# Kernel tuning notes

Measured on AMD Instinct MI355X. Metric: run time of the kernel, lower is better.

The kernel has to match this reference:

```python
import jax, jax.numpy as jnp
import numpy as np

B, S, D = 2, 2048, 1024
H = 16
HD = D // H  # 64
SCALE = HD ** -0.5


def setup_inputs() -> dict:
    key = jax.random.key(0)
    k1, k2, k3 = jax.random.split(key, 3)
    x = jax.random.normal(k1, (B, S, D), dtype=jnp.float32)
    w_qkv = jax.random.normal(k2, (D, 3 * D), dtype=jnp.float32) * (D ** -0.5)
    w_out = jax.random.normal(k3, (D, D), dtype=jnp.float32) * (D ** -0.5)
    return {"x": x, "w_qkv": w_qkv, "w_out": w_out}


def reference(x, w_qkv, w_out):
    batch, seq, hidden = x.shape
    qkv = jnp.einsum('bsd,de->bse', x, w_qkv)  # (B,S,3D)
    q, k, v = jnp.split(qkv, 3, axis=-1)
    # (B,H,S,HD)
    q = q.reshape(batch, seq, H, HD).transpose(0, 2, 1, 3)
    k = k.reshape(batch, seq, H, HD).transpose(0, 2, 1, 3)
    v = v.reshape(batch, seq, H, HD).transpose(0, 2, 1, 3)
    # full (B,H,S,S) scores, as in the original module
    scores = jnp.einsum('bhqd,bhkd->bhqk', q, k) * SCALE
    causal = jnp.tril(jnp.ones((seq, seq), dtype=bool))
    scores = jnp.where(causal[None, None], scores, -jnp.inf)
    attn = jax.nn.softmax(scores, axis=-1)
    out = jnp.einsum('bhqk,bhkd->bhqd', attn, v)
    out = out.transpose(0, 2, 1, 3).reshape(batch, seq, hidden)
    return jnp.einsum('bsd,de->bse', out, w_out)
```

## Files before the change

kernel.cpp:

```cpp
#include <hip/hip_runtime.h>
#include <hip/hip_bf16.h>
#include <stdint.h>

typedef unsigned short u16;
typedef unsigned int u32;
typedef __attribute__((ext_vector_type(8))) short short8;
typedef __attribute__((ext_vector_type(4))) short short4e;
typedef __attribute__((ext_vector_type(4))) float f32x4;
typedef __attribute__((ext_vector_type(16))) float f32x16;

constexpr int CB = 2, CS = 2048, CD = 1024, CH = 16, CHD = 64;
constexpr float SC2 = 0.125f * 1.44269504088896f;
constexpr float DEFER_THR = 11.0f;

__device__ __forceinline__ u16 f2bf(float f) {
    unsigned u = __float_as_uint(f);
    u += 0x7fffu + ((u >> 16) & 1u);
    return (u16)(u >> 16);
}

#if __has_builtin(__builtin_amdgcn_exp2f)
#define EXP2F(x) __builtin_amdgcn_exp2f(x)
#else
#define EXP2F(x) exp2f(x)
#endif

__device__ __forceinline__ u32 pkbf(float a, float b) {
    u32 r;
    asm("v_cvt_pk_bf16_f32 %0, %1, %2" : "=v"(r) : "v"(a), "v"(b));
    return r;
}

__global__ __launch_bounds__(256) void cvt_x(const float* __restrict__ X, u16* __restrict__ Y) {
    const int i = (blockIdx.x * 256 + threadIdx.x) * 8;
    const float4 v0 = *(const float4*)(X + i);
    const float4 v1 = *(const float4*)(X + i + 4);
    short8 r;
    r[0] = (short)f2bf(v0.x); r[1] = (short)f2bf(v0.y);
    r[2] = (short)f2bf(v0.z); r[3] = (short)f2bf(v0.w);
    r[4] = (short)f2bf(v1.x); r[5] = (short)f2bf(v1.y);
    r[6] = (short)f2bf(v1.z); r[7] = (short)f2bf(v1.w);
    *(short8*)(Y + i) = r;
}

__global__ __launch_bounds__(256) void txw(const float* __restrict__ W, u16* __restrict__ Bt,
                                           int ldw) {
    __shared__ u16 T[64][80];
    const int t = threadIdx.x;
    const int n0 = blockIdx.x * 64, k0 = blockIdx.y * 64;
    const int r = t >> 4, c4 = (t & 15) * 4;
#pragma unroll
    for (int p = 0; p < 4; ++p) {
        const int kr = r + p * 16;
        const float4 v = *(const float4*)(W + (size_t)(k0 + kr) * ldw + n0 + c4);
        T[c4 + 0][kr] = f2bf(v.x); T[c4 + 1][kr] = f2bf(v.y);
        T[c4 + 2][kr] = f2bf(v.z); T[c4 + 3][kr] = f2bf(v.w);
    }
    __syncthreads();
    const int rr = t >> 2, cc = (t & 3) * 16;
    const short8 a = *(const short8*)((const char*)&T[0][0] + rr * 160 + cc * 2);
    const short8 b = *(const short8*)((const char*)&T[0][0] + rr * 160 + cc * 2 + 16);
    u16* dst = Bt + (size_t)(n0 + rr) * 1024 + k0 + cc;
    *(short8*)dst = a;
    *(short8*)(dst + 8) = b;
}

__global__ __launch_bounds__(256) void gemm_mfma(
    const u16* __restrict__ A, const u16* __restrict__ Bt, int mode,
    u16* __restrict__ Qws, u16* __restrict__ Kws, u16* __restrict__ Vtws,
    float* __restrict__ Cf)
{
    __shared__ u16 SB[2][8192];
    const int tid = threadIdx.x;
    const int w = tid >> 6, lane = tid & 63;
    const int l15 = lane & 15, l4 = lane >> 4;
    const int wr = w >> 1, wc = w & 1;
    const int n0 = blockIdx.x * 128, m0 = blockIdx.y * 128;

    f32x4 acc[4][4];
    const f32x4 zf = {0.f, 0.f, 0.f, 0.f};
#pragma unroll
    for (int i = 0; i < 4; ++i)
#pragma unroll
        for (int j = 0; j < 4; ++j) acc[i][j] = zf;

#define GEMM_STAGE(BUF, K0)                                                     \
    {                                                                           \
        _Pragma("unroll")                                                       \
        for (int it = 0; it < 4; ++it) {                                        \
            const int c = tid + it * 256;                                       \
            const u16* src;                                                     \
            if (c < 512) { const int row = c >> 2, cs = c & 3;                  \
                src = A + (size_t)(m0 + row) * 1024 + (K0) + cs * 8; }          \
            else { const int c2 = c - 512; const int row = c2 >> 2, cs = c2 & 3;\
                src = Bt + (size_t)(n0 + row) * 1024 + (K0) + cs * 8; }         \
            __builtin_amdgcn_global_load_lds(                                   \
                (const __attribute__((address_space(1))) unsigned int*)src,     \
                (__attribute__((address_space(3))) unsigned int*)&SB[BUF][c*8], \
                16, 0, 0);                                                      \
        }                                                                       \
    }

    GEMM_STAGE(0, 0);
    __syncthreads();

    for (int t = 0; t < 32; ++t) {
        const int cur = t & 1;
        if (t < 31) GEMM_STAGE(cur ^ 1, (t + 1) * 32);

        const u16* Al = &SB[cur][0];
        const u16* Bl = &SB[cur][4096];
        short8 a[4], b[4];
#pragma unroll
        for (int i = 0; i < 4; ++i)
            a[i] = *(const short8*)(Al + (wr * 64 + i * 16 + l15) * 32 + l4 * 8);
#pragma unroll
        for (int j = 0; j < 4; ++j)
            b[j] = *(const short8*)(Bl + (wc * 64 + j * 16 + l15) * 32 + l4 * 8);
        __builtin_amdgcn_s_setprio(1);
#pragma unroll
        for (int i = 0; i < 4; ++i)
#pragma unroll
            for (int j = 0; j < 4; ++j)
                acc[i][j] = __builtin_amdgcn_mfma_f32_16x16x32_bf16(a[i], b[j], acc[i][j], 0, 0, 0);
        __builtin_amdgcn_s_setprio(0);
        __syncthreads();
    }

    if (mode == 1) {
#pragma unroll
        for (int i = 0; i < 4; ++i)
#pragma unroll
            for (int j = 0; j < 4; ++j)
#pragma unroll
                for (int r = 0; r < 4; ++r)
                    Cf[(size_t)(m0 + wr * 64 + i * 16 + l4 * 4 + r) * 1024 +
                       n0 + wc * 64 + j * 16 + l15] = acc[i][j][r];
    } else {
        const int e0 = n0 + wc * 64;
        const int which = e0 >> 10;
        const int h = (e0 >> 6) & 15;
        const int b = m0 >> 11;
        const int sbase = (m0 & 2047) + wr * 64;
        if (which == 2) {
#pragma unroll
            for (int i = 0; i < 4; ++i)
#pragma unroll
                for (int j = 0; j < 4; ++j) {
                    const int hd = j * 16 + l15;
                    const int s4 = sbase + i * 16 + l4 * 4;
                    short4e p;
                    p[0] = (short)f2bf(acc[i][j][0]); p[1] = (short)f2bf(acc[i][j][1]);
                    p[2] = (short)f2bf(acc[i][j][2]); p[3] = (short)f2bf(acc[i][j][3]);
                    *(short4e*)(Vtws + ((size_t)(b * 16 + h) * 64 + hd) * 2048 + s4) = p;
                }
        } else {
            u16* dst = which ? Kws : Qws;
            const float qsc = which ? 1.0f : SC2;
#pragma unroll
            for (int i = 0; i < 4; ++i)
#pragma unroll
                for (int j = 0; j < 4; ++j)
#pragma unroll
                    for (int r = 0; r < 4; ++r) {
                        const int s = sbase + i * 16 + l4 * 4 + r;
                        dst[((size_t)(b * 16 + h) * 2048 + s) * 64 + j * 16 + l15] =
                            f2bf(acc[i][j][r] * qsc);
                    }
        }
    }
#undef GEMM_STAGE
}

__global__ __launch_bounds__(64, 4) void attn_nolds(
    const u16* __restrict__ Qg, const u16* __restrict__ Kg,
    const u16* __restrict__ Vtg, u16* __restrict__ Og)
{
    const int lane = threadIdx.x;
    const int l31 = lane & 31, hi = lane >> 5;
    const int bid = blockIdx.x;
    const int bh = bid & 31;
    const int qchunk = 63 - (bid >> 5);
    const int q0 = qchunk * 32;
    const int qrow = q0 + l31;

    const u16* Qp = Qg + (size_t)bh * CS * CHD;
    const u16* Kp = Kg + (size_t)bh * CS * CHD;
    const u16* Vp = Vtg + (size_t)bh * CHD * CS;

    short8 qf[4];
#pragma unroll
    for (int c = 0; c < 4; ++c)
        qf[c] = *(const short8*)(Qp + (size_t)qrow * 64 + c * 16 + hi * 8);

    f32x16 o0, o1;
#pragma unroll
    for (int r = 0; r < 16; ++r) { o0[r] = 0.f; o1[r] = 0.f; }
    float m_run = -1e30f, l_run = 0.f;

    const int nkt = (qchunk >> 1) + 1;

    for (int kt = 0; kt < nkt; ++kt) {
        const int k0 = kt * 64;
        const bool edge = (k0 + 63 > q0);
        const bool do_hi = (k0 + 32 <= q0 + 31);

        const u16* Kb = Kp + (size_t)(k0 + l31) * 64 + hi * 8;
        f32x16 s0, s1;
#pragma unroll
        for (int r = 0; r < 16; ++r) s0[r] = 0.f;
        __builtin_amdgcn_s_setprio(1);
#pragma unroll
        for (int c = 0; c < 4; ++c) {
            const short8 kf = *(const short8*)(Kb + c * 16);
            s0 = __builtin_amdgcn_mfma_f32_32x32x16_bf16(kf, qf[c], s0, 0, 0, 0);
        }
        if (do_hi) {
#pragma unroll
            for (int r = 0; r < 16; ++r) s1[r] = 0.f;
#pragma unroll
            for (int c = 0; c < 4; ++c) {
                const short8 kf = *(const short8*)(Kb + 32 * 64 + c * 16);
                s1 = __builtin_amdgcn_mfma_f32_32x32x16_bf16(kf, qf[c], s1, 0, 0, 0);
            }
        }
        __builtin_amdgcn_s_setprio(0);

        float pmax = -1e30f;
#pragma unroll
        for (int r = 0; r < 16; ++r) {
            float a0 = s0[r];
            if (edge) {
                const int koff = (r & 3) + 8 * (r >> 2) + 4 * hi;
                if (k0 + koff > qrow) a0 = -1e30f;
            }
            s0[r] = a0;
            pmax = fmaxf(pmax, a0);
        }
        if (do_hi) {
#pragma unroll
            for (int r = 0; r < 16; ++r) {
                float a1 = s1[r];
                if (edge) {
                    const int koff = (r & 3) + 8 * (r >> 2) + 4 * hi;
                    if (k0 + 32 + koff > qrow) a1 = -1e30f;
                }
                s1[r] = a1;
                pmax = fmaxf(pmax, a1);
            }
        }
        pmax = fmaxf(pmax, __shfl_xor(pmax, 32));

        if (!__all(pmax - m_run <= DEFER_THR)) {
            const float mn = fmaxf(m_run, pmax);
            const float al = EXP2F(m_run - mn);
            l_run *= al;
            m_run = mn;
#pragma unroll
            for (int r = 0; r < 16; ++r) {
                const int qq = (r & 3) + 8 * (r >> 2) + 4 * hi;
                const float av = __shfl(al, qq);
                o0[r] *= av; o1[r] *= av;
            }
        }

        float lsum = 0.f;
#pragma unroll
        for (int r = 0; r < 16; ++r) {
            const float p0 = EXP2F(s0[r] - m_run);
            s0[r] = p0; lsum += p0;
        }
        if (do_hi) {
#pragma unroll
            for (int r = 0; r < 16; ++r) {
                const float p1 = EXP2F(s1[r] - m_run);
                s1[r] = p1; lsum += p1;
            }
        }
        lsum += __shfl_xor(lsum, 32);
        l_run += lsum;

        const u16* Vb  = Vp + (size_t)l31 * CS + k0 + hi * 8;
        const u16* Vb2 = Vb + (size_t)32 * CS;
#define PV_STEP(KS, SV)                                                          \
        {                                                                        \
            const int rb = ((KS) & 1) * 8;                                       \
            u32 w0 = pkbf(SV[rb + 0], SV[rb + 1]);                               \
            u32 w1 = pkbf(SV[rb + 2], SV[rb + 3]);                               \
            u32 w2 = pkbf(SV[rb + 4], SV[rb + 5]);                               \
            u32 w3 = pkbf(SV[rb + 6], SV[rb + 7]);                               \
            asm("v_permlane32_swap_b32 %0, %1" : "+v"(w0), "+v"(w2));            \
            asm("v_permlane32_swap_b32 %0, %1" : "+v"(w1), "+v"(w3));            \
            union { u32 uw[4]; short8 v; } pu;                                   \
            pu.uw[0] = w0; pu.uw[1] = w1; pu.uw[2] = w2; pu.uw[3] = w3;          \
            const short8 pa = pu.v;                                              \
            const short8 v0 = *(const short8*)(Vb  + (KS) * 16);                 \
            const short8 v1 = *(const short8*)(Vb2 + (KS) * 16);                 \
            __builtin_amdgcn_s_setprio(1);                                       \
            o0 = __builtin_amdgcn_mfma_f32_32x32x16_bf16(pa, v0, o0, 0, 0, 0);   \
            o1 = __builtin_amdgcn_mfma_f32_32x32x16_bf16(pa, v1, o1, 0, 0, 0);   \
            __builtin_amdgcn_s_setprio(0);                                       \
        }
        PV_STEP(0, s0)
        PV_STEP(1, s0)
        if (do_hi) {
            PV_STEP(2, s1)
            PV_STEP(3, s1)
        }
#undef PV_STEP
    }

    const float invl = 1.f / l_run;
    const int b = bh >> 4, h = bh & 15;
#pragma unroll
    for (int g = 0; g < 4; ++g)
#pragma unroll
        for (int c = 0; c < 4; ++c) {
            const int qq = 8 * g + 4 * hi + c;
            const float av = __shfl(invl, qq);
            u16* dst = Og + ((size_t)(b * CS + q0 + qq)) * CD + h * 64 + l31;
            dst[0]  = f2bf(o0[g * 4 + c] * av);
            dst[32] = f2bf(o1[g * 4 + c] * av);
        }
}

extern "C" void kernel_launch(void* const* d_in, const int* in_sizes, int n_in,
                              void* d_out, int out_size, void* d_ws, size_t ws_size,
                              hipStream_t stream)
{
    const float* x     = (const float*)d_in[0];
    const float* w_qkv = (const float*)d_in[1];
    const float* w_out = (const float*)d_in[2];
    float* out = (float*)d_out;

    u16* xb    = (u16*)d_ws;
    u16* wqkvT = xb    + (size_t)4096 * 1024;
    u16* woutT = wqkvT + (size_t)3072 * 1024;
    u16* Qws   = woutT + (size_t)1024 * 1024;
    u16* Kws   = Qws   + (size_t)32 * 2048 * 64;
    u16* Vtws  = Kws   + (size_t)32 * 2048 * 64;
    u16* Ob    = Vtws  + (size_t)32 * 2048 * 64;

    cvt_x<<<2048, 256, 0, stream>>>(x, xb);
    txw<<<dim3(48, 16), 256, 0, stream>>>(w_qkv, wqkvT, 3072);
    txw<<<dim3(16, 16), 256, 0, stream>>>(w_out, woutT, 1024);

    gemm_mfma<<<dim3(24, 32), 256, 0, stream>>>(xb, wqkvT, 0, Qws, Kws, Vtws, nullptr);
    attn_nolds<<<2048, 64, 0, stream>>>(Qws, Kws, Vtws, Ob);
    gemm_mfma<<<dim3(8, 32), 256, 0, stream>>>(Ob, woutT, 1, nullptr, nullptr, nullptr, out);
}
```

Baseline: 233.0 us.

## Split causal attention into KV segments with LDS-shared K/V and combine pass

Replaces the one-wave-per-32-query attention kernel with 4-wave blocks covering 128 queries. These blocks stage K and V tiles through double-buffered, XOR-swizzled LDS so all four waves share each load. Long query tiles are split into segments of up to 8 KV tiles to balance causal work across blocks. Partial outputs and running max/sum go to workspace and are merged by a new combine kernel. The aim is less redundant global K/V traffic and better load balance, at the cost of an extra launch, partial-result traffic and bf16 rounding of the unnormalized partials.

```diff
diff --git a/kernel.cpp b/kernel.cpp
--- a/kernel.cpp
+++ b/kernel.cpp
@@ -17,6 +17,9 @@
     unsigned u = __float_as_uint(f);
     u += 0x7fffu + ((u >> 16) & 1u);
     return (u16)(u >> 16);
+}
+__device__ __forceinline__ float bf2f(short s) {
+    return __uint_as_float(((u32)(unsigned short)s) << 16);
 }
 
 #if __has_builtin(__builtin_amdgcn_exp2f)
@@ -172,21 +175,36 @@
 #undef GEMM_STAGE
 }
 
-__global__ __launch_bounds__(64, 4) void attn_nolds(
+__global__ __launch_bounds__(256, 4) void attn_seg(
     const u16* __restrict__ Qg, const u16* __restrict__ Kg,
-    const u16* __restrict__ Vtg, u16* __restrict__ Og)
+    const u16* __restrict__ Vtg, u16* __restrict__ Og,
+    u16* __restrict__ Opart, float* __restrict__ Oml)
 {
-    const int lane = threadIdx.x;
+    __shared__ u16 KV[2][8192];
+
+    static const int jt_of_u[40] = {0,1,2,3, 4,4, 5,5, 6,6, 7,7,
+                                    8,8,8, 9,9,9, 10,10,10, 11,11,11,
+                                    12,12,12,12, 13,13,13,13, 14,14,14,14, 15,15,15,15};
+    static const int seg_of_u[40] = {0,0,0,0, 0,1, 0,1, 0,1, 0,1,
+                                     0,1,2, 0,1,2, 0,1,2, 0,1,2,
+                                     0,1,2,3, 0,1,2,3, 0,1,2,3, 0,1,2,3};
+
+    const int tid = threadIdx.x;
+    const int w = tid >> 6, lane = tid & 63;
     const int l31 = lane & 31, hi = lane >> 5;
     const int bid = blockIdx.x;
+    const int u = 39 - (bid >> 5);
     const int bh = bid & 31;
-    const int qchunk = 63 - (bid >> 5);
-    const int q0 = qchunk * 32;
-    const int qrow = q0 + l31;
+    const int jt = jt_of_u[u], seg = seg_of_u[u];
+    const int t0 = seg * 8;
+    const int tmax = 2 * jt + 2;
+    const int t1 = (tmax < t0 + 8) ? tmax : (t0 + 8);
 
     const u16* Qp = Qg + (size_t)bh * CS * CHD;
     const u16* Kp = Kg + (size_t)bh * CS * CHD;
     const u16* Vp = Vtg + (size_t)bh * CHD * CS;
+    const int q0w = jt * 128 + w * 32;
+    const int qrow = q0w + l31;
 
     short8 qf[4];
 #pragma unroll
@@ -198,130 +216,252 @@
     for (int r = 0; r < 16; ++r) { o0[r] = 0.f; o1[r] = 0.f; }
     float m_run = -1e30f, l_run = 0.f;
 
-    const int nkt = (qchunk >> 1) + 1;
-
-    for (int kt = 0; kt < nkt; ++kt) {
+    short8 stg[4];
+#define ATTN_ISSUE(K0)                                                           \
+    {                                                                            \
+        _Pragma("unroll")                                                        \
+        for (int it = 0; it < 4; ++it) {                                         \
+            const int c = tid + it * 256;                                        \
+            const int ob = c * 16;                                               \
+            const u16* src;                                                      \
+            if (ob < 8192) { const int row = ob >> 7, cs = (ob >> 4) & 7;        \
+                src = Kp + (size_t)((K0) + row) * 64 + cs * 8; }                 \
+            else { const int o2 = ob - 8192; const int row = o2 >> 7,            \
+                cs = (o2 >> 4) & 7;                                              \
+                src = Vp + (size_t)row * CS + (K0) + cs * 8; }                   \
+            stg[it] = *(const short8*)src;                                       \
+        }                                                                        \
+    }
+#define ATTN_WRITE(BUF)                                                          \
+    {                                                                            \
+        _Pragma("unroll")                                                        \
+        for (int it = 0; it < 4; ++it) {                                         \
+            const int c = tid + it * 256;                                        \
+            const int ob = c * 16;                                               \
+            int db;                                                              \
+            if (ob < 8192) { const int row = ob >> 7; db = ob ^ ((row & 7) << 4); } \
+            else { const int o2 = ob - 8192; const int row = o2 >> 7;            \
+                db = 8192 + (o2 ^ ((row & 7) << 4)); }                           \
+            *(short8*)((char*)&KV[BUF][0] + db) = stg[it];                       \
+        }                                                                        \
+    }
+
+    ATTN_ISSUE(t0 * 64);
+    ATTN_WRITE(0);
+    __syncthreads();
+
+    for (int kt = t0; kt < t1; ++kt) {
         const int k0 = kt * 64;
-        const bool edge = (k0 + 63 > q0);
-        const bool do_hi = (k0 + 32 <= q0 + 31);
-
-        const u16* Kb = Kp + (size_t)(k0 + l31) * 64 + hi * 8;
-        f32x16 s0, s1;
-#pragma unroll
-        for (int r = 0; r < 16; ++r) s0[r] = 0.f;
-        __builtin_amdgcn_s_setprio(1);
-#pragma unroll
-        for (int c = 0; c < 4; ++c) {
-            const short8 kf = *(const short8*)(Kb + c * 16);
-            s0 = __builtin_amdgcn_mfma_f32_32x32x16_bf16(kf, qf[c], s0, 0, 0, 0);
-        }
-        if (do_hi) {
-#pragma unroll
-            for (int r = 0; r < 16; ++r) s1[r] = 0.f;
+        const int cur = (kt - t0) & 1;
+        if (kt + 1 < t1) ATTN_ISSUE((kt + 1) * 64);
+
+        if (k0 <= q0w + 31) {
+            const char* Kl = (const char*)&KV[cur][0];
+            const char* Vl = (const char*)&KV[cur][4096];
+            const bool edge = (k0 + 63 > q0w);
+            const bool do_hi = (k0 + 32 <= q0w + 31);
+
+            f32x16 s0, s1;
+#pragma unroll
+            for (int r = 0; r < 16; ++r) s0[r] = 0.f;
+            __builtin_amdgcn_s_setprio(1);
 #pragma unroll
             for (int c = 0; c < 4; ++c) {
-                const short8 kf = *(const short8*)(Kb + 32 * 64 + c * 16);
-                s1 = __builtin_amdgcn_mfma_f32_32x32x16_bf16(kf, qf[c], s1, 0, 0, 0);
-            }
-        }
-        __builtin_amdgcn_s_setprio(0);
-
-        float pmax = -1e30f;
-#pragma unroll
-        for (int r = 0; r < 16; ++r) {
-            float a0 = s0[r];
-            if (edge) {
-                const int koff = (r & 3) + 8 * (r >> 2) + 4 * hi;
-                if (k0 + koff > qrow) a0 = -1e30f;
-            }
-            s0[r] = a0;
-            pmax = fmaxf(pmax, a0);
-        }
-        if (do_hi) {
+                const int row = l31;
+                const short8 kf = *(const short8*)(Kl + row * 128 +
+                                    ((c * 32 + hi * 16) ^ ((row & 7) << 4)));
+                s0 = __builtin_amdgcn_mfma_f32_32x32x16_bf16(kf, qf[c], s0, 0, 0, 0);
+            }
+            if (do_hi) {
+#pragma unroll
+                for (int r = 0; r < 16; ++r) s1[r] = 0.f;
+#pragma unroll
+                for (int c = 0; c < 4; ++c) {
+                    const int row = 32 + l31;
+                    const short8 kf = *(const short8*)(Kl + row * 128 +
+                                        ((c * 32 + hi * 16) ^ ((row & 7) << 4)));
+                    s1 = __builtin_amdgcn_mfma_f32_32x32x16_bf16(kf, qf[c], s1, 0, 0, 0);
+                }
+            }
+            __builtin_amdgcn_s_setprio(0);
+
+            float pmax = -1e30f;
 #pragma unroll
             for (int r = 0; r < 16; ++r) {
-                float a1 = s1[r];
+                float a0 = s0[r];
                 if (edge) {
                     const int koff = (r & 3) + 8 * (r >> 2) + 4 * hi;
-                    if (k0 + 32 + koff > qrow) a1 = -1e30f;
-                }
-                s1[r] = a1;
-                pmax = fmaxf(pmax, a1);
-            }
+                    if (k0 + koff > qrow) a0 = -1e30f;
+                }
+                s0[r] = a0;
+                pmax = fmaxf(pmax, a0);
+            }
+            if (do_hi) {
+#pragma unroll
+                for (int r = 0; r < 16; ++r) {
+                    float a1 = s1[r];
+                    if (edge) {
+                        const int koff = (r & 3) + 8 * (r >> 2) + 4 * hi;
+                        if (k0 + 32 + koff > qrow) a1 = -1e30f;
+                    }
+                    s1[r] = a1;
+                    pmax = fmaxf(pmax, a1);
+                }
+            }
+            pmax = fmaxf(pmax, __shfl_xor(pmax, 32));
+
+            if (!__all(pmax - m_run <= DEFER_THR)) {
+                const float mn = fmaxf(m_run, pmax);
+                const float al = EXP2F(m_run - mn);
+                l_run *= al;
+                m_run = mn;
+#pragma unroll
+                for (int r = 0; r < 16; ++r) {
+                    const int qq = (r & 3) + 8 * (r >> 2) + 4 * hi;
+                    const float av = __shfl(al, qq);
+                    o0[r] *= av; o1[r] *= av;
+                }
+            }
+
+            float lsum = 0.f;
+#pragma unroll
+            for (int r = 0; r < 16; ++r) {
+                const float p0 = EXP2F(s0[r] - m_run);
+                s0[r] = p0; lsum += p0;
+            }
+            if (do_hi) {
+#pragma unroll
+                for (int r = 0; r < 16; ++r) {
+                    const float p1 = EXP2F(s1[r] - m_run);
+                    s1[r] = p1; lsum += p1;
+                }
+            }
+            lsum += __shfl_xor(lsum, 32);
+            l_run += lsum;
+
+#define PV_STEP(KS, SV)                                                          \
+            {                                                                    \
+                const int rb = ((KS) & 1) * 8;                                   \
+                u32 w0 = pkbf(SV[rb + 0], SV[rb + 1]);                           \
+                u32 w1 = pkbf(SV[rb + 2], SV[rb + 3]);                           \
+                u32 w2 = pkbf(SV[rb + 4], SV[rb + 5]);                           \
+                u32 w3 = pkbf(SV[rb + 6], SV[rb + 7]);                           \
+                asm("v_permlane32_swap_b32 %0, %1" : "+v"(w0), "+v"(w2));        \
+                asm("v_permlane32_swap_b32 %0, %1" : "+v"(w1), "+v"(w3));        \
+                union { u32 uw[4]; short8 v; } pu;                               \
+                pu.uw[0] = w0; pu.uw[1] = w1; pu.uw[2] = w2; pu.uw[3] = w3;      \
+                const short8 pa = pu.v;                                          \
+                const int vr0 = l31, vr1 = 32 + l31;                             \
+                const short8 v0 = *(const short8*)(Vl + vr0 * 128 +              \
+                                    (((KS) * 32 + hi * 16) ^ ((vr0 & 7) << 4))); \
+                const short8 v1 = *(const short8*)(Vl + vr1 * 128 +              \
+                                    (((KS) * 32 + hi * 16) ^ ((vr1 & 7) << 4))); \
+                __builtin_amdgcn_s_setprio(1);                                   \
+                o0 = __builtin_amdgcn_mfma_f32_32x32x16_bf16(pa, v0, o0, 0, 0, 0);\
+                o1 = __builtin_amdgcn_mfma_f32_32x32x16_bf16(pa, v1, o1, 0, 0, 0);\
+                __builtin_amdgcn_s_setprio(0);                                   \
+            }
+            PV_STEP(0, s0)
+            PV_STEP(1, s0)
+            if (do_hi) {
+                PV_STEP(2, s1)
+                PV_STEP(3, s1)
+            }
+#undef PV_STEP
         }
-        pmax = fmaxf(pmax, __shfl_xor(pmax, 32));
-
-        if (!__all(pmax - m_run <= DEFER_THR)) {
-            const float mn = fmaxf(m_run, pmax);
-            const float al = EXP2F(m_run - mn);
-            l_run *= al;
-            m_run = mn;
-#pragma unroll
-            for (int r = 0; r < 16; ++r) {
-                const int qq = (r & 3) + 8 * (r >> 2) + 4 * hi;
-                const float av = __shfl(al, qq);
-                o0[r] *= av; o1[r] *= av;
-            }
+
+        if (kt + 1 < t1) ATTN_WRITE(cur ^ 1);
+        __syncthreads();
+    }
+
+    if (jt < 4) {
+        const float invl = 1.f / l_run;
+        const int b = bh >> 4, h = bh & 15;
+#pragma unroll
+        for (int g = 0; g < 4; ++g)
+#pragma unroll
+            for (int c = 0; c < 4; ++c) {
+                const int qq = 8 * g + 4 * hi + c;
+                const float av = __shfl(invl, qq);
+                u16* dst = Og + ((size_t)(bh >> 4) * CS + jt * 128 + w * 32 + qq) * CD
+                             + (bh & 15) * 64 + l31;
+                dst[0]  = f2bf(o0[g * 4 + c] * av);
+                dst[32] = f2bf(o1[g * 4 + c] * av);
+            }
+        (void)0;
+    } else {
+        const int slot = bh * 36 + (u - 4);
+        u16* pd = Opart + ((size_t)slot * 128 + w * 32) * 64;
+#pragma unroll
+        for (int g = 0; g < 4; ++g)
+#pragma unroll
+            for (int c = 0; c < 4; ++c) {
+                const int qq = 8 * g + 4 * hi + c;
+                pd[qq * 64 + l31]      = f2bf(o0[g * 4 + c]);
+                pd[qq * 64 + 32 + l31] = f2bf(o1[g * 4 + c]);
+            }
+        if (lane < 32) {
+            const size_t mi = ((size_t)slot * 128 + w * 32 + l31) * 2;
+            Oml[mi]     = m_run;
+            Oml[mi + 1] = l_run;
         }
-
-        float lsum = 0.f;
-#pragma unroll
-        for (int r = 0; r < 16; ++r) {
-            const float p0 = EXP2F(s0[r] - m_run);
-            s0[r] = p0; lsum += p0;
+    }
+#undef ATTN_ISSUE
+#undef ATTN_WRITE
+}
+
+__global__ __launch_bounds__(256) void attn_combine(
+    const u16* __restrict__ Opart, const float* __restrict__ Oml,
+    u16* __restrict__ Og)
+{
+    static const int ub[16] = {0,1,2,3,4,6,8,10,12,15,18,21,24,28,32,36};
+    const int jt = 4 + blockIdx.x;
+    const int bh = blockIdx.y;
+    const int tid = threadIdx.x;
+    const int r = tid >> 1, half = tid & 1;
+    const int segs = (jt + 4) >> 2;
+    const int slot0 = bh * 36 + ub[jt] - 4;
+
+    float acc[32];
+#pragma unroll
+    for (int k = 0; k < 32; ++k) acc[k] = 0.f;
+    float M = -1e30f, L = 0.f;
+
+    for (int i = 0; i < segs; ++i) {
+        const int slot = slot0 + i;
+        const float mi = Oml[((size_t)slot * 128 + r) * 2];
+        const float li = Oml[((size_t)slot * 128 + r) * 2 + 1];
+        float wi;
+        if (mi > M) {
+            const float sc = EXP2F(M - mi);
+#pragma unroll
+            for (int k = 0; k < 32; ++k) acc[k] *= sc;
+            L *= sc; M = mi; wi = 1.f;
+        } else {
+            wi = EXP2F(mi - M);
         }
-        if (do_hi) {
-#pragma unroll
-            for (int r = 0; r < 16; ++r) {
-                const float p1 = EXP2F(s1[r] - m_run);
-                s1[r] = p1; lsum += p1;
-            }
+        const u16* op = Opart + ((size_t)slot * 128 + r) * 64 + half * 32;
+#pragma unroll
+        for (int v = 0; v < 4; ++v) {
+            const short8 x = *(const short8*)(op + v * 8);
+#pragma unroll
+            for (int e = 0; e < 8; ++e)
+                acc[v * 8 + e] += wi * bf2f(x[e]);
         }
-        lsum += __shfl_xor(lsum, 32);
-        l_run += lsum;
-
-        const u16* Vb  = Vp + (size_t)l31 * CS + k0 + hi * 8;
-        const u16* Vb2 = Vb + (size_t)32 * CS;
-#define PV_STEP(KS, SV)                                                          \
-        {                                                                        \
-            const int rb = ((KS) & 1) * 8;                                       \
-            u32 w0 = pkbf(SV[rb + 0], SV[rb + 1]);                               \
-            u32 w1 = pkbf(SV[rb + 2], SV[rb + 3]);                               \
-            u32 w2 = pkbf(SV[rb + 4], SV[rb + 5]);                               \
-            u32 w3 = pkbf(SV[rb + 6], SV[rb + 7]);                               \
-            asm("v_permlane32_swap_b32 %0, %1" : "+v"(w0), "+v"(w2));            \
-            asm("v_permlane32_swap_b32 %0, %1" : "+v"(w1), "+v"(w3));            \
-            union { u32 uw[4]; short8 v; } pu;                                   \
-            pu.uw[0] = w0; pu.uw[1] = w1; pu.uw[2] = w2; pu.uw[3] = w3;          \
-            const short8 pa = pu.v;                                              \
-            const short8 v0 = *(const short8*)(Vb  + (KS) * 16);                 \
-            const short8 v1 = *(const short8*)(Vb2 + (KS) * 16);                 \
-            __builtin_amdgcn_s_setprio(1);                                       \
-            o0 = __builtin_amdgcn_mfma_f32_32x32x16_bf16(pa, v0, o0, 0, 0, 0);   \
-            o1 = __builtin_amdgcn_mfma_f32_32x32x16_bf16(pa, v1, o1, 0, 0, 0);   \
-            __builtin_amdgcn_s_setprio(0);                                       \
-        }
-        PV_STEP(0, s0)
-        PV_STEP(1, s0)
-        if (do_hi) {
-            PV_STEP(2, s1)
-            PV_STEP(3, s1)
-        }
-#undef PV_STEP
-    }
-
-    const float invl = 1.f / l_run;
+        L += wi * li;
+    }
+
+    const float inv = 1.f / L;
     const int b = bh >> 4, h = bh & 15;
-#pragma unroll
-    for (int g = 0; g < 4; ++g)
-#pragma unroll
-        for (int c = 0; c < 4; ++c) {
-            const int qq = 8 * g + 4 * hi + c;
-            const float av = __shfl(invl, qq);
-            u16* dst = Og + ((size_t)(b * CS + q0 + qq)) * CD + h * 64 + l31;
-            dst[0]  = f2bf(o0[g * 4 + c] * av);
-            dst[32] = f2bf(o1[g * 4 + c] * av);
-        }
+    const int q = jt * 128 + r;
+    u16* dst = Og + ((size_t)(b * CS + q)) * CD + h * 64 + half * 32;
+#pragma unroll
+    for (int v = 0; v < 4; ++v) {
+        short8 y;
+#pragma unroll
+        for (int e = 0; e < 8; ++e) y[e] = (short)f2bf(acc[v * 8 + e] * inv);
+        *(short8*)(dst + v * 8) = y;
+    }
 }
 
 extern "C" void kernel_launch(void* const* d_in, const int* in_sizes, int n_in,
@@ -340,12 +480,15 @@
     u16* Kws   = Qws   + (size_t)32 * 2048 * 64;
     u16* Vtws  = Kws   + (size_t)32 * 2048 * 64;
     u16* Ob    = Vtws  + (size_t)32 * 2048 * 64;
+    u16* Opart = Ob    + (size_t)4096 * 1024;
+    float* Oml = (float*)(Opart + (size_t)1152 * 128 * 64);
 
     cvt_x<<<2048, 256, 0, stream>>>(x, xb);
     txw<<<dim3(48, 16), 256, 0, stream>>>(w_qkv, wqkvT, 3072);
     txw<<<dim3(16, 16), 256, 0, stream>>>(w_out, woutT, 1024);
 
     gemm_mfma<<<dim3(24, 32), 256, 0, stream>>>(xb, wqkvT, 0, Qws, Kws, Vtws, nullptr);
-    attn_nolds<<<2048, 64, 0, stream>>>(Qws, Kws, Vtws, Ob);
+    attn_seg<<<1280, 256, 0, stream>>>(Qws, Kws, Vtws, Ob, Opart, Oml);
+    attn_combine<<<dim3(12, 32), 256, 0, stream>>>(Opart, Oml, Ob);
     gemm_mfma<<<dim3(8, 32), 256, 0, stream>>>(Ob, woutT, 1, nullptr, nullptr, nullptr, out);
 }
```

New measurement: 225.0 us. 1.04x faster.
